# Performance work log

Measured on AMD Instinct MI355X. Metric: run time of the kernel, lower is better.

Reference implementation:

```python
import jax, jax.numpy as jnp
import numpy as np

NUM_CLASSES = 7
B = 14336
D = 512
H_KDE = 0.2          # sklearn KernelDensity(bandwidth=0.2, kernel='gaussian')
KERNEL_MUL = 2.0
KERNEL_NUM = 5
BN_EPS = 1e-5


def _pairwise_sqdist(a, b):
    # ||a_i - b_j||^2 via gram trick; avoids the [n,n,d] broadcast tensor the torch code builds
    an = jnp.sum(a * a, axis=-1)
    bn = jnp.sum(b * b, axis=-1)
    d2 = an[:, None] + bn[None, :] - 2.0 * (a @ b.T)
    return jnp.maximum(d2, 0.0)


def _multi_kernel(total):
    # sum of KERNEL_NUM Gaussian kernels, bandwidths 1.25 * 2^i (bandwidth=5 / 2^(5//2))
    d2 = _pairwise_sqdist(total, total)
    bw0 = 5.0 / (KERNEL_MUL ** (KERNEL_NUM // 2))
    k = jnp.zeros_like(d2)
    for i in range(KERNEL_NUM):  # small fixed loop, avoids [5,n,n] intermediate
        k = k + jnp.exp(-d2 / (bw0 * (KERNEL_MUL ** i)))
    return k


def _mmd(src, tgt):
    m = src.shape[0]
    k = _multi_kernel(jnp.concatenate([src, tgt], axis=0))
    return jnp.mean(k[:m, :m] + k[m:, m:] - k[:m, m:] - k[m:, :m])


def _kde_weight(class_feats):
    # sklearn gaussian KDE: log p(x_i) = logsumexp_j(-||x_i-x_j||^2 / (2 h^2)) - log m - (d/2) log(2 pi h^2)
    # volume v = sum_i 1 / log p(x_i); weight = 1 / (v + 1e-5)
    C, m, d = class_feats.shape
    log_norm = -0.5 * d * jnp.log(2.0 * jnp.pi * (H_KDE ** 2)) - jnp.log(jnp.float32(m))

    def one(f):
        d2 = _pairwise_sqdist(f, f)
        logp = jax.nn.logsumexp(-d2 / (2.0 * (H_KDE ** 2)), axis=1) + log_norm
        return jnp.sum(1.0 / logp)

    v = jax.vmap(one)(class_feats)
    return 1.0 / (v + 1e-5)


def setup_inputs() -> dict:
    key = jax.random.key(0)
    k1, k2 = jax.random.split(key)
    fea = jax.random.normal(k1, (B, D), dtype=jnp.float32) * 0.05
    W_fc = jax.random.normal(k2, (NUM_CLASSES, D), dtype=jnp.float32) * 0.02
    gamma = jnp.ones((NUM_CLASSES,), dtype=jnp.float32)
    beta = jnp.zeros((NUM_CLASSES,), dtype=jnp.float32)
    # balanced, contiguous class blocks so per-class splits are static reshapes
    targets = jnp.repeat(jnp.arange(NUM_CLASSES, dtype=jnp.int32), B // NUM_CLASSES)
    return {"fea": fea, "W_fc": W_fc, "gamma": gamma, "beta": beta, "targets": targets}


def reference(fea, W_fc, gamma, beta, targets):
    Bn, d = fea.shape
    C = NUM_CLASSES
    m = Bn // C

    # out = BatchNorm1d(fc(fea)) in train mode (biased batch stats)
    logits = fea @ W_fc.T                              # [B, C]
    mu = jnp.mean(logits, axis=0)
    var = jnp.var(logits, axis=0)
    out = gamma * (logits - mu) / jnp.sqrt(var + BN_EPS) + beta

    # split_feature_makeLD with balanced contiguous targets -> static reshape
    cf = fea.reshape(C, m, d)                          # [C, m, D]

    # KDE density weights: computed on detached numpy features in the original -> stop_gradient
    w = jax.lax.stop_gradient(_kde_weight(cf))         # [C]

    def per_class(i):
        src = cf[i]
        # remove_element concatenates classes 0..i-1, i+1..C-1 in order;
        # first m rows of that = class 0 (class 1 when i == 0)
        tgt = cf[jnp.where(i > 0, 0, 1)]
        return _mmd(src, tgt)

    losses = jax.vmap(per_class)(jnp.arange(C))        # [C]
    affinity_loss = -jnp.sum(losses * w)
    return (out, affinity_loss)
```

## Files before the change

### kernel.cpp

```cpp
#include <hip/hip_runtime.h>

#define B_ROWS 14336
#define D_DIM  512
#define C_CLS  7
#define M_CLS  2048

typedef __attribute__((ext_vector_type(4))) float f32x4;

#define FP8_SCALE 64.0f
#define INV_2S2   (2.0f / 4096.0f)

typedef const __attribute__((address_space(1))) char gchar_t;
typedef __attribute__((address_space(3))) char lchar_t;

__device__ __forceinline__ void gload16(const char* g, char* l) {
  __builtin_amdgcn_global_load_lds((gchar_t*)g, (lchar_t*)l, 16, 0, 0);
}

__global__ __launch_bounds__(256) void k_prep(const float* __restrict__ fea,
                                              const float* __restrict__ W,
                                              char* __restrict__ f8p,
                                              float* __restrict__ an,
                                              float* __restrict__ logits,
                                              float* __restrict__ zb) {
  int t = threadIdx.x, wave = t >> 6, lane = t & 63;
  if (blockIdx.x == 0 && t < 64) zb[t] = 0.f;
  __shared__ char lrow[16 * 528];

  int r0 = blockIdx.x * 16;
#pragma unroll
  for (int k = 0; k < 4; ++k) {
    int rl = wave * 4 + k;
    int row = r0 + rl;
    const float4* fr4 = (const float4*)(fea + (size_t)row * D_DIM);
    float4 v0 = fr4[lane * 2], v1 = fr4[lane * 2 + 1];

    float p[8];
#pragma unroll
    for (int c = 0; c < 7; ++c) {
      const float4* w4 = (const float4*)(W + c * D_DIM);
      float4 q0 = w4[lane * 2], q1 = w4[lane * 2 + 1];
      p[c] = v0.x * q0.x + v0.y * q0.y + v0.z * q0.z + v0.w * q0.w +
             v1.x * q1.x + v1.y * q1.y + v1.z * q1.z + v1.w * q1.w;
    }
    p[7] = v0.x * v0.x + v0.y * v0.y + v0.z * v0.z + v0.w * v0.w +
           v1.x * v1.x + v1.y * v1.y + v1.z * v1.z + v1.w * v1.w;

#pragma unroll
    for (int c = 0; c < 8; ++c) {
      p[c] += __shfl_xor(p[c], 1);
      p[c] += __shfl_xor(p[c], 2);
      p[c] += __shfl_xor(p[c], 4);
    }
    int v = lane & 7;
    float y = p[0];
    y = (v == 1) ? p[1] : y;
    y = (v == 2) ? p[2] : y;
    y = (v == 3) ? p[3] : y;
    y = (v == 4) ? p[4] : y;
    y = (v == 5) ? p[5] : y;
    y = (v == 6) ? p[6] : y;
    y = (v == 7) ? p[7] : y;
    y += __shfl_xor(y, 8);
    y += __shfl_xor(y, 16);
    y += __shfl_xor(y, 32);
    if (lane < 7) logits[row * 7 + lane] = y;
    else if (lane == 7) an[row] = y;

    int w0 = __builtin_amdgcn_cvt_pk_fp8_f32(v0.x * FP8_SCALE, v0.y * FP8_SCALE, 0, 0);
    w0     = __builtin_amdgcn_cvt_pk_fp8_f32(v0.z * FP8_SCALE, v0.w * FP8_SCALE, w0, 1);
    int w1 = __builtin_amdgcn_cvt_pk_fp8_f32(v1.x * FP8_SCALE, v1.y * FP8_SCALE, 0, 0);
    w1     = __builtin_amdgcn_cvt_pk_fp8_f32(v1.z * FP8_SCALE, v1.w * FP8_SCALE, w1, 1);
    *(int2*)&lrow[rl * 528 + lane * 8] = make_int2(w0, w1);
  }
  __syncthreads();
  int4* outp = (int4*)f8p + (size_t)blockIdx.x * 512;
#pragma unroll
  for (int pi = 0; pi < 2; ++pi) {
    int idx = pi * 256 + t;
    int kp = idx >> 6, l = idx & 63;
    int sr = l & 15, qk = l >> 4;
    int2 lo = *(const int2*)&lrow[sr * 528 + kp * 64 + qk * 8];
    int2 hi = *(const int2*)&lrow[sr * 528 + kp * 64 + 32 + qk * 8];
    outp[idx] = make_int4(lo.x, lo.y, hi.x, hi.y);
  }
}

__global__ __launch_bounds__(512, 2) void k_gram(const char* __restrict__ f8p,
                                                 const float* __restrict__ an,
                                                 const float* __restrict__ logits,
                                                 float* __restrict__ S,
                                                 float* __restrict__ rs_part,
                                                 float* __restrict__ S1,
                                                 float* __restrict__ S2,
                                                 float* __restrict__ aff) {
  int x = blockIdx.x & 7, u = blockIdx.x >> 3;
  int t = threadIdx.x, lane = t & 63, wave = t >> 6;
  if (blockIdx.x == 0 && t == 0) aff[0] = 0.f;

  if (u == 80) {
    if (x >= 7) return;
    int c = x, seg = wave;
    int r0 = seg * 1792;
    float s1 = 0.f, s2 = 0.f;
    for (int j = lane; j < 1792; j += 64) {
      float v = logits[(size_t)(r0 + j) * 7 + c];
      s1 += v;
      s2 += v * v;
    }
#pragma unroll
    for (int o = 1; o < 64; o <<= 1) {
      s1 += __shfl_xor(s1, o);
      s2 += __shfl_xor(s2, o);
    }
    if (lane == 0) { atomicAdd(&S1[c], s1); atomicAdd(&S2[c], s2); }
    return;
  }

  int cls1, cls2, ti, tj, Sidx;
  bool self;
  if (x < 7 && u < 36) {
    int a = 0, r = u;
    while (r > a) { r -= a + 1; ++a; }
    ti = a; tj = r;
    cls1 = x; cls2 = x; Sidx = x; self = true;
  } else {
    int j;
    if (x < 7) j = x * 44 + (u - 36);
    else { if (u >= 76) return; j = 308 + u; }
    int p = j >> 6, t64 = j & 63;
    ti = t64 >> 3; tj = t64 & 7;
    cls1 = p + 1; cls2 = 0; Sidx = 7 + p; self = false;
  }

  __shared__ char ldsA[2][16384];
  __shared__ char ldsB[2][16384];
  __shared__ float bacc[8];

  int R0 = cls1 * 2048 + ti * 256;
  int C0 = cls2 * 2048 + tj * 256;

  const char* gA0 = f8p + ((size_t)(R0 >> 4) + wave * 2)     * 8192 + lane * 16;
  const char* gA1 = f8p + ((size_t)(R0 >> 4) + wave * 2 + 1) * 8192 + lane * 16;
  const char* gB0 = f8p + ((size_t)(C0 >> 4) + wave * 2)     * 8192 + lane * 16;
  const char* gB1 = f8p + ((size_t)(C0 >> 4) + wave * 2 + 1) * 8192 + lane * 16;

#define STAGE(kt_, bf_)                                                      \
  do {                                                                       \
    gload16(gA0 + (kt_) * 1024, &ldsA[bf_][(wave * 2) * 1024 + lane * 16]);  \
    gload16(gA1 + (kt_) * 1024, &ldsA[bf_][(wave * 2 + 1) * 1024 + lane * 16]); \
    gload16(gB0 + (kt_) * 1024, &ldsB[bf_][(wave * 2) * 1024 + lane * 16]);  \
    gload16(gB1 + (kt_) * 1024, &ldsB[bf_][(wave * 2 + 1) * 1024 + lane * 16]); \
  } while (0)

  int wr = wave >> 2, wc = wave & 3;
  int q = lane >> 4, s = lane & 15;

  f32x4 acc[8][4];
#pragma unroll
  for (int i = 0; i < 8; ++i)
#pragma unroll
    for (int j = 0; j < 4; ++j)
      acc[i][j] = (f32x4){0.f, 0.f, 0.f, 0.f};

  STAGE(0, 0);
  __syncthreads();

#pragma unroll 1
  for (int kt = 0; kt < 8; ++kt) {
    int cur = kt & 1;
    if (kt < 7) {
      STAGE(kt + 1, cur ^ 1);
      asm volatile("s_waitcnt vmcnt(4)" ::: "memory");
    } else {
      asm volatile("s_waitcnt vmcnt(0)" ::: "memory");
    }
    __builtin_amdgcn_s_barrier();
    asm volatile("" ::: "memory");
    const char* LA = &ldsA[cur][(wr * 8) * 1024 + lane * 16];
    const char* LB = &ldsB[cur][(wc * 4) * 1024 + lane * 16];
    longlong2 a_[8], bb_[4];
#pragma unroll
    for (int i = 0; i < 8; ++i) a_[i] = *(const longlong2*)(LA + i * 1024);
#pragma unroll
    for (int j = 0; j < 4; ++j) bb_[j] = *(const longlong2*)(LB + j * 1024);
    asm volatile("s_waitcnt lgkmcnt(0)" ::: "memory");
    __builtin_amdgcn_sched_barrier(0);
    __builtin_amdgcn_s_setprio(1);
#pragma unroll
    for (int i = 0; i < 8; ++i)
#pragma unroll
      for (int j = 0; j < 4; ++j)
        acc[i][j] = __builtin_amdgcn_mfma_f32_16x16x32_fp8_fp8(
            a_[i].x, bb_[j].x, acc[i][j], 0, 0, 0);
#pragma unroll
    for (int i = 0; i < 8; ++i)
#pragma unroll
      for (int j = 0; j < 4; ++j)
        acc[i][j] = __builtin_amdgcn_mfma_f32_16x16x32_fp8_fp8(
            a_[i].y, bb_[j].y, acc[i][j], 0, 0, 0);
    __builtin_amdgcn_s_setprio(0);
    __builtin_amdgcn_s_barrier();
    asm volatile("" ::: "memory");
  }
#undef STAGE

  bool dg = self && (ti == tj);
  bool mirror = self && (ti > tj);
  float blockAcc = 0.f;
  float colAcc[4] = {0.f, 0.f, 0.f, 0.f};
  float anB_[4];
#pragma unroll
  for (int j = 0; j < 4; ++j) anB_[j] = an[C0 + wc * 64 + j * 16 + s];

#pragma unroll
  for (int i = 0; i < 8; ++i) {
    f32x4 anA_ = *(const f32x4*)&an[R0 + wr * 128 + i * 16 + q * 4];
#pragma unroll
    for (int rg = 0; rg < 4; ++rg) {
      int rl = wr * 128 + i * 16 + q * 4 + rg;
      float aA = anA_[rg];
      float rowAcc = 0.f;
#pragma unroll
      for (int j = 0; j < 4; ++j) {
        int cl = wc * 64 + j * 16 + s;
        float g = acc[i][j][rg];
        float d2 = fmaxf(aA + anB_[j] - g * INV_2S2, 0.f);
        if (dg && rl == cl) d2 = 0.f;
        float e1 = __expf(-0.05f * d2);
        float e2 = e1 * e1, e4 = e2 * e2, e8 = e4 * e4, e16 = e8 * e8;
        blockAcc += e1 + e2 + e4 + e8 + e16;
        if (self) {
          float ek = __expf(-12.5f * d2);
          rowAcc += ek;
          if (mirror) colAcc[j] += ek;
        }
      }
      if (self) {
        rowAcc += __shfl_xor(rowAcc, 1);
        rowAcc += __shfl_xor(rowAcc, 2);
        rowAcc += __shfl_xor(rowAcc, 4);
        rowAcc += __shfl_xor(rowAcc, 8);
        if (s == 0)
          rs_part[(size_t)(R0 + rl) * 48 + tj * 4 + wc] = rowAcc;
      }
    }
  }
  if (mirror) {
#pragma unroll
    for (int j = 0; j < 4; ++j) {
      float v = colAcc[j];
      v += __shfl_xor(v, 16);
      v += __shfl_xor(v, 32);
      if (q == 0)
        rs_part[(size_t)(C0 + wc * 64 + j * 16 + s) * 48 + 32 + ti * 2 + wr] = v;
    }
    blockAcc *= 2.f;
  }
#pragma unroll
  for (int o = 1; o < 64; o <<= 1) blockAcc += __shfl_xor(blockAcc, o);
  if (lane == 0) bacc[wave] = blockAcc;
  __syncthreads();
  if (t == 0) {
    float sB = 0.f;
#pragma unroll
    for (int w = 0; w < 8; ++w) sB += bacc[w];
    atomicAdd(&S[Sidx], sB);
  }
}

__global__ __launch_bounds__(1024) void k_final(const float* __restrict__ logits,
                                                const float* __restrict__ S1,
                                                const float* __restrict__ S2,
                                                const float* __restrict__ gamma,
                                                const float* __restrict__ beta,
                                                const float* __restrict__ rs_part,
                                                const float* __restrict__ S,
                                                float* __restrict__ out) {
  int b = blockIdx.x, t = threadIdx.x;
  if (b < 98) {
    int idx = b * 1024 + t;
    int row = idx / 7;
    int c = idx - row * 7;
    float mu = S1[c] * (1.f / 14336.f);
    float var = S2[c] * (1.f / 14336.f) - mu * mu;
    out[idx] = gamma[c] * (logits[idx] - mu) * rsqrtf(var + 1e-5f) + beta[c];
    return;
  }
  int c = b - 98;
  const float LOG_NORM = 345.9110632f;
  float v = 0.f;
  for (int i = t; i < M_CLS; i += 1024) {
    int bi = i >> 8;
    const float* rp = rs_part + (size_t)(c * M_CLS + i) * 48;
    float rsum = 0.f;
    int nd = 4 * bi + 4;
    for (int k = 0; k < nd; ++k) rsum += rp[k];
    for (int k = 34 + 2 * bi; k < 48; ++k) rsum += rp[k];
    v += 1.f / (logf(rsum) + LOG_NORM);
  }
#pragma unroll
  for (int o = 1; o < 64; o <<= 1) v += __shfl_xor(v, o);
  __shared__ float r[16];
  if ((t & 63) == 0) r[t >> 6] = v;
  __syncthreads();
  if (t == 0) {
    float vs = 0.f;
#pragma unroll
    for (int w = 0; w < 16; ++w) vs += r[w];
    float w = 1.f / (vs + 1e-5f);
    const float inv_m2 = 1.0f / ((float)M_CLS * (float)M_CLS);
    float Ssrc = S[c];
    float Stgt = (c > 0) ? S[0] : S[1];
    float X    = (c > 0) ? S[6 + c] : S[7];
    float mmd = (Ssrc + Stgt - 2.f * X) * inv_m2;
    atomicAdd(&out[100352], -mmd * w);
  }
}

extern "C" void kernel_launch(void* const* d_in, const int* in_sizes, int n_in,
                              void* d_out, int out_size, void* d_ws, size_t ws_size,
                              hipStream_t stream) {
  const float* fea   = (const float*)d_in[0];
  const float* W_fc  = (const float*)d_in[1];
  const float* gamma = (const float*)d_in[2];
  const float* beta  = (const float*)d_in[3];
  float* out = (float*)d_out;

  char* ws = (char*)d_ws;
  char* f8p = ws;
  float* fbase   = (float*)(ws + 7340032);
  float* an      = fbase;
  float* logits  = fbase + 14336;
  float* zb      = fbase + 114688;
  float* S1      = zb;
  float* S2      = zb + 7;
  float* S       = zb + 16;
  float* rs_part = fbase + 114752;

  k_prep <<<896, 256, 0, stream>>>(fea, W_fc, f8p, an, logits, zb);
  k_gram <<<648, 512, 0, stream>>>(f8p, an, logits, S, rs_part, S1, S2,
                                   out + 100352);
  k_final<<<105, 1024, 0, stream>>>(logits, S1, S2, gamma, beta, rs_part, S, out);
}
```

Measured before the change: 196.0 us.

## Interleave LDS reads, global prefetch and MFMA in four phases per K-step

Restructures the fp8 MFMA main loop so each K-tile is split into four sub-phases. Each phase loads two A fragments from LDS and issues 16 MFMAs, and the next tile's global-to-LDS loads are issued between phases. Waits on global loads are deferred to the end of the iteration. The goal is to overlap LDS reads and global prefetch with matrix math and to reduce register pressure from holding all eight A fragments. The cost is more barriers per iteration and a risk of pipeline stalls.

```diff
diff --git a/kernel.cpp b/kernel.cpp
--- a/kernel.cpp
+++ b/kernel.cpp
@@ -145,14 +145,6 @@
   const char* gB0 = f8p + ((size_t)(C0 >> 4) + wave * 2)     * 8192 + lane * 16;
   const char* gB1 = f8p + ((size_t)(C0 >> 4) + wave * 2 + 1) * 8192 + lane * 16;
 
-#define STAGE(kt_, bf_)                                                      \
-  do {                                                                       \
-    gload16(gA0 + (kt_) * 1024, &ldsA[bf_][(wave * 2) * 1024 + lane * 16]);  \
-    gload16(gA1 + (kt_) * 1024, &ldsA[bf_][(wave * 2 + 1) * 1024 + lane * 16]); \
-    gload16(gB0 + (kt_) * 1024, &ldsB[bf_][(wave * 2) * 1024 + lane * 16]);  \
-    gload16(gB1 + (kt_) * 1024, &ldsB[bf_][(wave * 2 + 1) * 1024 + lane * 16]); \
-  } while (0)
-
   int wr = wave >> 2, wc = wave & 3;
   int q = lane >> 4, s = lane & 15;
 
@@ -163,47 +155,78 @@
     for (int j = 0; j < 4; ++j)
       acc[i][j] = (f32x4){0.f, 0.f, 0.f, 0.f};
 
-  STAGE(0, 0);
+  gload16(gA0, &ldsA[0][(wave * 2) * 1024 + lane * 16]);
+  gload16(gA1, &ldsA[0][(wave * 2 + 1) * 1024 + lane * 16]);
+  gload16(gB0, &ldsB[0][(wave * 2) * 1024 + lane * 16]);
+  gload16(gB1, &ldsB[0][(wave * 2 + 1) * 1024 + lane * 16]);
   __syncthreads();
+
+#define MM16(A0_, A1_, I0_, I1_)                                              \
+  do {                                                                        \
+    asm volatile("s_waitcnt lgkmcnt(0)" ::: "memory");                        \
+    __builtin_amdgcn_sched_barrier(0);                                        \
+    __builtin_amdgcn_s_setprio(1);                                            \
+    _Pragma("unroll")                                                         \
+    for (int j_ = 0; j_ < 4; ++j_)                                            \
+      acc[I0_][j_] = __builtin_amdgcn_mfma_f32_16x16x32_fp8_fp8(              \
+          A0_.x, bb[j_].x, acc[I0_][j_], 0, 0, 0);                            \
+    _Pragma("unroll")                                                         \
+    for (int j_ = 0; j_ < 4; ++j_)                                            \
+      acc[I1_][j_] = __builtin_amdgcn_mfma_f32_16x16x32_fp8_fp8(              \
+          A1_.x, bb[j_].x, acc[I1_][j_], 0, 0, 0);                            \
+    _Pragma("unroll")                                                         \
+    for (int j_ = 0; j_ < 4; ++j_)                                            \
+      acc[I0_][j_] = __builtin_amdgcn_mfma_f32_16x16x32_fp8_fp8(              \
+          A0_.y, bb[j_].y, acc[I0_][j_], 0, 0, 0);                            \
+    _Pragma("unroll")                                                         \
+    for (int j_ = 0; j_ < 4; ++j_)                                            \
+      acc[I1_][j_] = __builtin_amdgcn_mfma_f32_16x16x32_fp8_fp8(              \
+          A1_.y, bb[j_].y, acc[I1_][j_], 0, 0, 0);                            \
+    __builtin_amdgcn_s_setprio(0);                                            \
+  } while (0)
 
 #pragma unroll 1
   for (int kt = 0; kt < 8; ++kt) {
     int cur = kt & 1;
+    const char* LA = &ldsA[cur][(wr * 8) * 1024 + lane * 16];
+    const char* LB = &ldsB[cur][(wc * 4) * 1024 + lane * 16];
+    longlong2 a0, a1, bb[4];
+    a0 = *(const longlong2*)(LA);
+    a1 = *(const longlong2*)(LA + 1024);
+#pragma unroll
+    for (int j = 0; j < 4; ++j) bb[j] = *(const longlong2*)(LB + j * 1024);
     if (kt < 7) {
-      STAGE(kt + 1, cur ^ 1);
-      asm volatile("s_waitcnt vmcnt(4)" ::: "memory");
-    } else {
-      asm volatile("s_waitcnt vmcnt(0)" ::: "memory");
+      int nb = cur ^ 1;
+      gload16(gA0 + (kt + 1) * 1024, &ldsA[nb][(wave * 2) * 1024 + lane * 16]);
+      gload16(gA1 + (kt + 1) * 1024, &ldsA[nb][(wave * 2 + 1) * 1024 + lane * 16]);
+    }
+    MM16(a0, a1, 0, 1);
+    a0 = *(const longlong2*)(LA + 2 * 1024);
+    a1 = *(const longlong2*)(LA + 3 * 1024);
+    if (kt < 7) {
+      int nb = cur ^ 1;
+      gload16(gB0 + (kt + 1) * 1024, &ldsB[nb][(wave * 2) * 1024 + lane * 16]);
+      gload16(gB1 + (kt + 1) * 1024, &ldsB[nb][(wave * 2 + 1) * 1024 + lane * 16]);
     }
     __builtin_amdgcn_s_barrier();
     asm volatile("" ::: "memory");
-    const char* LA = &ldsA[cur][(wr * 8) * 1024 + lane * 16];
-    const char* LB = &ldsB[cur][(wc * 4) * 1024 + lane * 16];
-    longlong2 a_[8], bb_[4];
-#pragma unroll
-    for (int i = 0; i < 8; ++i) a_[i] = *(const longlong2*)(LA + i * 1024);
-#pragma unroll
-    for (int j = 0; j < 4; ++j) bb_[j] = *(const longlong2*)(LB + j * 1024);
-    asm volatile("s_waitcnt lgkmcnt(0)" ::: "memory");
-    __builtin_amdgcn_sched_barrier(0);
-    __builtin_amdgcn_s_setprio(1);
-#pragma unroll
-    for (int i = 0; i < 8; ++i)
-#pragma unroll
-      for (int j = 0; j < 4; ++j)
-        acc[i][j] = __builtin_amdgcn_mfma_f32_16x16x32_fp8_fp8(
-            a_[i].x, bb_[j].x, acc[i][j], 0, 0, 0);
-#pragma unroll
-    for (int i = 0; i < 8; ++i)
-#pragma unroll
-      for (int j = 0; j < 4; ++j)
-        acc[i][j] = __builtin_amdgcn_mfma_f32_16x16x32_fp8_fp8(
-            a_[i].y, bb_[j].y, acc[i][j], 0, 0, 0);
-    __builtin_amdgcn_s_setprio(0);
+    MM16(a0, a1, 2, 3);
+    a0 = *(const longlong2*)(LA + 4 * 1024);
+    a1 = *(const longlong2*)(LA + 5 * 1024);
     __builtin_amdgcn_s_barrier();
     asm volatile("" ::: "memory");
-  }
-#undef STAGE
+    MM16(a0, a1, 4, 5);
+    a0 = *(const longlong2*)(LA + 6 * 1024);
+    a1 = *(const longlong2*)(LA + 7 * 1024);
+    __builtin_amdgcn_s_barrier();
+    asm volatile("" ::: "memory");
+    MM16(a0, a1, 6, 7);
+    if (kt < 7)
+      asm volatile("s_waitcnt vmcnt(0)" ::: "memory");
+    __builtin_amdgcn_s_barrier();
+    asm volatile("" ::: "memory");
+  }
+#undef MM16
 
   bool dg = self && (ti == tj);
   bool mirror = self && (ti > tj);
```

Measured after the change: 186.3 us. -4.9%, faster.
